# Kernel optimization log

Hardware: AMD Instinct MI355X
Metric: run time of the kernel (lower is better)

Reference implementation:

```python
import jax, jax.numpy as jnp
import numpy as np

N = 25000
E = 400000
IN_DIM = 512
H = 8
D = 64
ALPHA = 0.2  # leaky relu negative slope


def setup_inputs() -> dict:
    key = jax.random.key(0)
    k1, k2, k3, k4, k5 = jax.random.split(key, 5)
    inputs = jax.random.normal(k1, (N, IN_DIM), dtype=jnp.float32)
    src = jax.random.randint(k2, (E,), 0, N)
    dst = jnp.arange(E) % N  # every node has E/N inbound edges -> normalizer > 0
    # parameters (xavier-normal-ish scale)
    W = jax.random.normal(k3, (H * D, IN_DIM), dtype=jnp.float32) * (1.414 * (2.0 / (IN_DIM + H * D)) ** 0.5)
    attn_l = jax.random.normal(k4, (H, D), dtype=jnp.float32) * (1.414 * (2.0 / (D + 1)) ** 0.5)
    attn_r = jax.random.normal(k5, (H, D), dtype=jnp.float32) * (1.414 * (2.0 / (D + 1)) ** 0.5)
    return {"inputs": inputs, "W": W, "attn_l": attn_l, "attn_r": attn_r, "src": src, "dst": dst}


def reference(inputs, W, attn_l, attn_r, src, dst):
    # node projection: [N, H, D]
    ft = (inputs @ W.T).reshape(N, H, D)
    # per-node attention scalars per head: [N, H]
    a1 = jnp.einsum('nhd,hd->nh', ft, attn_l)
    a2 = jnp.einsum('nhd,hd->nh', ft, attn_r)
    # edge scores with leaky relu: [E, H]
    e = a1[src] + a2[dst]
    e = jnp.where(e > 0, e, ALPHA * e)
    # numerically stable edge softmax over incoming edges of each dst node
    emax = jax.ops.segment_max(e, dst, num_segments=N)  # [N, H]
    scores = jnp.exp(e - emax[dst])                      # [E, H]
    z = jax.ops.segment_sum(scores, dst, num_segments=N)  # [N, H]
    # weighted scatter-sum aggregation: [N, H, D]
    msg = ft[src] * scores[:, :, None]                   # [E, H, D]
    agg = jax.ops.segment_sum(msg, dst, num_segments=N)
    return agg / z[:, :, None]
```

## Files before the change

kernel.cpp:

```cpp
#include <hip/hip_runtime.h>
#include <math.h>

#define N_NODES 25000
#define E_EDGES 400000
#define IN_DIM  512
#define H_HEADS 8
#define D_HEAD  64
#define OUT_DIM 512
#define ALPHA   0.2f
#define EPN     16

typedef __attribute__((ext_vector_type(8))) short short8;
typedef __attribute__((ext_vector_type(4))) short short4v;
typedef __attribute__((ext_vector_type(4))) float floatx4;

__device__ __forceinline__ unsigned short f2bf(float x) {
    unsigned u = __float_as_uint(x);
    u += 0x7fffu + ((u >> 16) & 1u);
    return (unsigned short)(u >> 16);
}

__device__ __forceinline__ void gl_lds16(const unsigned short* g, unsigned short* l) {
    __builtin_amdgcn_global_load_lds((const __attribute__((address_space(1))) unsigned int*)g,
                                     (__attribute__((address_space(3))) unsigned int*)l,
                                     16, 0, 0);
}

#define W8 (OUT_DIM * IN_DIM / 8)

__global__ __launch_bounds__(256) void cvt_w(const float* __restrict__ W,
                                             unsigned short* __restrict__ Wbf) {
    int idx = blockIdx.x * 256 + threadIdx.x;
    if (idx >= W8) return;
    const float* s = W + (size_t)idx * 8;
    float4 v0 = ((const float4*)s)[0], v1 = ((const float4*)s)[1];
    short8 o;
    o[0] = f2bf(v0.x); o[1] = f2bf(v0.y); o[2] = f2bf(v0.z); o[3] = f2bf(v0.w);
    o[4] = f2bf(v1.x); o[5] = f2bf(v1.y); o[6] = f2bf(v1.z); o[7] = f2bf(v1.w);
    *(short8*)(Wbf + (size_t)idx * 8) = o;
}

#define GBM 64
#define GBK 32
#define NKSTEP (IN_DIM / GBK)

__global__ __launch_bounds__(512) void gemm_bf(const float* __restrict__ A,
                                               const unsigned short* __restrict__ Wbf,
                                               const float* __restrict__ attn_l,
                                               const float* __restrict__ attn_r,
                                               unsigned short* __restrict__ ftb,
                                               float* __restrict__ a1g,
                                               float* __restrict__ a2g) {
    __shared__ unsigned short As[2][GBM * GBK];
    __shared__ unsigned short Bs[2][OUT_DIM * GBK];

    const int t = threadIdx.x;
    const int wave = t >> 6;
    const int lane = t & 63;
    const int lr = lane & 15;
    const int lq = lane >> 4;
    const int mb = blockIdx.x * GBM;

    const int srow = lane >> 2;
    const int schunk = (lane & 3) * 8;
    const unsigned short* gB = Wbf + (size_t)(wave * 64 + srow) * IN_DIM + schunk;

    const int arow = t >> 3;
    const int acol = (t & 7) * 4;
    int ar_g = mb + arow;
    if (ar_g >= N_NODES) ar_g = N_NODES - 1;
    const float* gA = A + (size_t)ar_g * IN_DIM + acol;
    const int a_off = arow * GBK + acol;

    floatx4 acc[4][4] = {};

    {
        #pragma unroll
        for (int s = 0; s < 4; ++s)
            gl_lds16(gB + (size_t)s * 16 * IN_DIM, &Bs[0][wave * 64 * GBK + s * 16 * GBK]);
        floatx4 av = __builtin_nontemporal_load((const floatx4*)gA);
        short4v o;
        o[0] = f2bf(av[0]); o[1] = f2bf(av[1]); o[2] = f2bf(av[2]); o[3] = f2bf(av[3]);
        *(short4v*)&As[0][a_off] = o;
    }
    __syncthreads();

    int cur = 0;
    for (int ks = 0; ks < NKSTEP; ++ks) {
        const int nxt = cur ^ 1;
        const bool more = (ks + 1 < NKSTEP);
        const int k1 = (ks + 1) * GBK;

        floatx4 av;
        if (more) {
            #pragma unroll
            for (int s = 0; s < 4; ++s)
                gl_lds16(gB + (size_t)s * 16 * IN_DIM + k1,
                         &Bs[nxt][wave * 64 * GBK + s * 16 * GBK]);
            av = __builtin_nontemporal_load((const floatx4*)(gA + k1));
        }

        const unsigned short* a_rd = &As[cur][lr * GBK + lq * 8];
        const unsigned short* b_rd = &Bs[cur][(wave * 64 + lr) * GBK + lq * 8];
        short8 af[4], bq[4];
        #pragma unroll
        for (int i = 0; i < 4; ++i) af[i] = *(const short8*)(a_rd + i * 16 * GBK);
        #pragma unroll
        for (int j = 0; j < 4; ++j) bq[j] = *(const short8*)(b_rd + j * 16 * GBK);
        #pragma unroll
        for (int i = 0; i < 4; ++i)
            #pragma unroll
            for (int j = 0; j < 4; ++j)
                acc[i][j] = __builtin_amdgcn_mfma_f32_16x16x32_bf16(af[i], bq[j], acc[i][j], 0, 0, 0);

        if (more) {
            short4v o;
            o[0] = f2bf(av[0]); o[1] = f2bf(av[1]); o[2] = f2bf(av[2]); o[3] = f2bf(av[3]);
            *(short4v*)&As[nxt][a_off] = o;
        }
        __syncthreads();
        cur = nxt;
    }

    const int h = wave;
    float al[4], ar[4];
    #pragma unroll
    for (int j = 0; j < 4; ++j) {
        al[j] = attn_l[h * D_HEAD + j * 16 + lr];
        ar[j] = attn_r[h * D_HEAD + j * 16 + lr];
    }
    #pragma unroll
    for (int i = 0; i < 4; ++i) {
        #pragma unroll
        for (int r = 0; r < 4; ++r) {
            float s1 = 0.f, s2 = 0.f;
            #pragma unroll
            for (int j = 0; j < 4; ++j) {
                s1 += acc[i][j][r] * al[j];
                s2 += acc[i][j][r] * ar[j];
            }
            #pragma unroll
            for (int off = 1; off < 16; off <<= 1) {
                s1 += __shfl_xor(s1, off, 64);
                s2 += __shfl_xor(s2, off, 64);
            }
            if (lr == 0) {
                int n = mb + i * 16 + lq * 4 + r;
                if (n < N_NODES) {
                    a1g[h * N_NODES + n] = s1;
                    a2g[h * N_NODES + n] = s2;
                }
            }
        }
    }

    #pragma unroll
    for (int i = 0; i < 4; ++i) {
        #pragma unroll
        for (int j = 0; j < 4; ++j) {
            const int nrow = mb + i * 16 + lq * 4;
            const int col = wave * 64 + j * 16 + lr;
            #pragma unroll
            for (int r = 0; r < 4; ++r) {
                int nn = nrow + r;
                if (nn < N_NODES)
                    ftb[(size_t)nn * OUT_DIM + col] = f2bf(acc[i][j][r]);
            }
        }
    }
}

__global__ __launch_bounds__(256, 3) void agg_kernel(const unsigned short* __restrict__ ftb,
                                                     const float* __restrict__ a1T,
                                                     const float* __restrict__ a2T,
                                                     const int* __restrict__ src,
                                                     float* __restrict__ out) {
    __shared__ float s_w[32][EPN + 1];
    __shared__ int   s_is[32][EPN + 1];

    const int h     = blockIdx.x & 7;
    const int chunk = blockIdx.x >> 3;
    const int t = threadIdx.x;
    const int nd = t >> 3;
    const int l  = t & 7;
    const int v  = chunk * 32 + nd;
    const bool valid = v < N_NODES;
    const int vc = valid ? v : N_NODES - 1;

    {
        int s0 = src[vc + l * N_NODES];
        int s1 = src[vc + (l + 8) * N_NODES];
        float a2v = a2T[h * N_NODES + vc];
        float x0 = a1T[h * N_NODES + s0] + a2v;
        float x1 = a1T[h * N_NODES + s1] + a2v;
        float e0 = x0 > 0.f ? x0 : ALPHA * x0;
        float e1 = x1 > 0.f ? x1 : ALPHA * x1;
        float m = fmaxf(e0, e1);
        #pragma unroll
        for (int off = 1; off < 8; off <<= 1) m = fmaxf(m, __shfl_xor(m, off, 64));
        float w0 = __expf(e0 - m), w1 = __expf(e1 - m);
        float z = w0 + w1;
        #pragma unroll
        for (int off = 1; off < 8; off <<= 1) z += __shfl_xor(z, off, 64);
        float iz = 1.f / z;
        s_w[nd][l]      = w0 * iz;
        s_w[nd][l + 8]  = w1 * iz;
        s_is[nd][l]     = s0;
        s_is[nd][l + 8] = s1;
    }
    __syncthreads();

    float wl[EPN];
    const unsigned short* ap[EPN];
    const unsigned short* fp = ftb + h * D_HEAD + l * 8;
    #pragma unroll
    for (int j = 0; j < EPN; ++j) {
        wl[j] = s_w[nd][j];
        ap[j] = fp + (size_t)s_is[nd][j] * OUT_DIM;
    }
    uint4 q[EPN];
    #pragma unroll
    for (int j = 0; j < EPN; ++j) q[j] = *(const uint4*)ap[j];

    float acc[8] = {};
    #pragma unroll
    for (int j = 0; j < EPN; ++j) {
        float wj = wl[j];
        acc[0] += wj * __uint_as_float(q[j].x << 16);
        acc[1] += wj * __uint_as_float(q[j].x & 0xffff0000u);
        acc[2] += wj * __uint_as_float(q[j].y << 16);
        acc[3] += wj * __uint_as_float(q[j].y & 0xffff0000u);
        acc[4] += wj * __uint_as_float(q[j].z << 16);
        acc[5] += wj * __uint_as_float(q[j].z & 0xffff0000u);
        acc[6] += wj * __uint_as_float(q[j].w << 16);
        acc[7] += wj * __uint_as_float(q[j].w & 0xffff0000u);
    }
    if (valid) {
        floatx4* op = (floatx4*)(out + (size_t)v * OUT_DIM + h * D_HEAD + l * 8);
        floatx4 o0 = {acc[0], acc[1], acc[2], acc[3]};
        floatx4 o1 = {acc[4], acc[5], acc[6], acc[7]};
        __builtin_nontemporal_store(o0, op + 0);
        __builtin_nontemporal_store(o1, op + 1);
    }
}

extern "C" void kernel_launch(void* const* d_in, const int* in_sizes, int n_in,
                              void* d_out, int out_size, void* d_ws, size_t ws_size,
                              hipStream_t stream) {
    const float* inputs = (const float*)d_in[0];
    const float* W      = (const float*)d_in[1];
    const float* attn_l = (const float*)d_in[2];
    const float* attn_r = (const float*)d_in[3];
    const int*   src    = (const int*)d_in[4];

    float* out = (float*)d_out;
    unsigned short* ftb = (unsigned short*)d_ws;
    unsigned short* Wbf = ftb + (size_t)N_NODES * IN_DIM;
    float* a1 = (float*)(Wbf + (size_t)OUT_DIM * IN_DIM);
    float* a2 = a1 + (size_t)N_NODES * H_HEADS;

    cvt_w<<<(W8 + 255) / 256, 256, 0, stream>>>(W, Wbf);

    gemm_bf<<<(N_NODES + GBM - 1) / GBM, 512, 0, stream>>>(inputs, Wbf, attn_l, attn_r,
                                                           ftb, a1, a2);

    agg_kernel<<<8 * ((N_NODES + 31) / 32), 256, 0, stream>>>(ftb, a1, a2, src, out);
}
```

Baseline: 186.7 us.

## Halve GEMM row tile and drop LDS double buffering for occupancy

```diff
diff --git a/kernel.cpp b/kernel.cpp
--- a/kernel.cpp
+++ b/kernel.cpp
@@ -40,7 +40,7 @@
     *(short8*)(Wbf + (size_t)idx * 8) = o;
 }
 
-#define GBM 64
+#define GBM 32
 #define GBK 32
 #define NKSTEP (IN_DIM / GBK)
 
@@ -51,8 +51,8 @@
                                                unsigned short* __restrict__ ftb,
                                                float* __restrict__ a1g,
                                                float* __restrict__ a2g) {
-    __shared__ unsigned short As[2][GBM * GBK];
-    __shared__ unsigned short Bs[2][OUT_DIM * GBK];
+    __shared__ unsigned short As[GBM * GBK];
+    __shared__ unsigned short Bs[OUT_DIM * GBK];
 
     const int t = threadIdx.x;
     const int wave = t >> 6;
@@ -61,9 +61,8 @@
     const int lq = lane >> 4;
     const int mb = blockIdx.x * GBM;
 
-    const int srow = lane >> 2;
-    const int schunk = (lane & 3) * 8;
-    const unsigned short* gB = Wbf + (size_t)(wave * 64 + srow) * IN_DIM + schunk;
+    const unsigned short* gB = Wbf + (size_t)(wave * 16 + (lane >> 2)) * IN_DIM + (lane & 3) * 8;
+    unsigned short* lB = Bs + wave * 512;
 
     const int arow = t >> 3;
     const int acol = (t & 7) * 4;
@@ -72,54 +71,33 @@
     const float* gA = A + (size_t)ar_g * IN_DIM + acol;
     const int a_off = arow * GBK + acol;
 
-    floatx4 acc[4][4] = {};
-
-    {
+    floatx4 acc[2][4] = {};
+    const unsigned short* a_rd = As + lr * GBK + lq * 8;
+    const unsigned short* b_rd = Bs + (wave * 64 + lr) * GBK + lq * 8;
+
+    for (int k0 = 0; k0 < IN_DIM; k0 += GBK) {
         #pragma unroll
         for (int s = 0; s < 4; ++s)
-            gl_lds16(gB + (size_t)s * 16 * IN_DIM, &Bs[0][wave * 64 * GBK + s * 16 * GBK]);
-        floatx4 av = __builtin_nontemporal_load((const floatx4*)gA);
-        short4v o;
-        o[0] = f2bf(av[0]); o[1] = f2bf(av[1]); o[2] = f2bf(av[2]); o[3] = f2bf(av[3]);
-        *(short4v*)&As[0][a_off] = o;
-    }
-    __syncthreads();
-
-    int cur = 0;
-    for (int ks = 0; ks < NKSTEP; ++ks) {
-        const int nxt = cur ^ 1;
-        const bool more = (ks + 1 < NKSTEP);
-        const int k1 = (ks + 1) * GBK;
-
-        floatx4 av;
-        if (more) {
-            #pragma unroll
-            for (int s = 0; s < 4; ++s)
-                gl_lds16(gB + (size_t)s * 16 * IN_DIM + k1,
-                         &Bs[nxt][wave * 64 * GBK + s * 16 * GBK]);
-            av = __builtin_nontemporal_load((const floatx4*)(gA + k1));
+            gl_lds16(gB + (size_t)s * 128 * IN_DIM + k0, lB + s * 4096);
+        if (t < 256) {
+            floatx4 av = *(const floatx4*)(gA + k0);
+            short4v o;
+            o[0] = f2bf(av[0]); o[1] = f2bf(av[1]); o[2] = f2bf(av[2]); o[3] = f2bf(av[3]);
+            *(short4v*)&As[a_off] = o;
         }
-
-        const unsigned short* a_rd = &As[cur][lr * GBK + lq * 8];
-        const unsigned short* b_rd = &Bs[cur][(wave * 64 + lr) * GBK + lq * 8];
-        short8 af[4], bq[4];
-        #pragma unroll
-        for (int i = 0; i < 4; ++i) af[i] = *(const short8*)(a_rd + i * 16 * GBK);
+        __syncthreads();
+
+        short8 af[2], bq[4];
+        #pragma unroll
+        for (int i = 0; i < 2; ++i) af[i] = *(const short8*)(a_rd + i * 16 * GBK);
         #pragma unroll
         for (int j = 0; j < 4; ++j) bq[j] = *(const short8*)(b_rd + j * 16 * GBK);
         #pragma unroll
-        for (int i = 0; i < 4; ++i)
+        for (int i = 0; i < 2; ++i)
             #pragma unroll
             for (int j = 0; j < 4; ++j)
                 acc[i][j] = __builtin_amdgcn_mfma_f32_16x16x32_bf16(af[i], bq[j], acc[i][j], 0, 0, 0);
-
-        if (more) {
-            short4v o;
-            o[0] = f2bf(av[0]); o[1] = f2bf(av[1]); o[2] = f2bf(av[2]); o[3] = f2bf(av[3]);
-            *(short4v*)&As[nxt][a_off] = o;
-        }
         __syncthreads();
-        cur = nxt;
     }
 
     const int h = wave;
@@ -130,7 +108,7 @@
         ar[j] = attn_r[h * D_HEAD + j * 16 + lr];
     }
     #pragma unroll
-    for (int i = 0; i < 4; ++i) {
+    for (int i = 0; i < 2; ++i) {
         #pragma unroll
         for (int r = 0; r < 4; ++r) {
             float s1 = 0.f, s2 = 0.f;
@@ -155,7 +133,7 @@
     }
 
     #pragma unroll
-    for (int i = 0; i < 4; ++i) {
+    for (int i = 0; i < 2; ++i) {
         #pragma unroll
         for (int j = 0; j < 4; ++j) {
             const int nrow = mb + i * 16 + lq * 4;
```

Result: faster. 178.6 us (-4.3%).
